# Performance work log

Hardware: AMD Instinct MI355X
Metric: run time of the kernel (lower is better)

## Reference

```python
import jax, jax.numpy as jnp
import numpy as np

# --- Instant-NGP hash-grid constants (from __init__ defaults) ---
T = 2 ** 19          # hash table size per level
NLEVELS = 16
F = 2                # features per level
L = 4                # dir positional-encoding frequencies
LEVELS = np.geomspace(16, 2048, NLEVELS, dtype=int)            # grid resolutions
PRIMES = jnp.array([1, 2654435761, 805459861], dtype=jnp.uint32)
FREQS = (2.0 ** np.arange(L)).astype(np.float32)
# corner c in 0..7 -> bit b_i = use ceil along dim i (matches torch corner order)
BITS = jnp.array([[(c >> i) & 1 for i in range(3)] for c in range(8)], dtype=bool)  # (8,3)


def _hash_encode(pos, table):
    """pos: (P,3) level-scaled positions; table: (T,F). Returns (P,F).
    Spatial hash + gather + trilinear interpolation (== grid_sample trick)."""
    fl = jnp.floor(pos)
    ce = jnp.ceil(pos)
    frac = pos - fl                                             # (P,3) in [0,1)
    corners = jnp.where(BITS[None], ce[:, None, :], fl[:, None, :]).astype(jnp.int32)  # (P,8,3)
    # uint32 wrap-around arithmetic matches torch int64 mod 2^19 (T is a power of 2)
    v = corners.astype(jnp.uint32) * PRIMES                     # (P,8,3)
    h = (v[..., 0] ^ v[..., 1] ^ v[..., 2]) & jnp.uint32(T - 1) # (P,8)
    cf = table[h]                                               # (P,8,F) irregular gather
    w = jnp.prod(jnp.where(BITS[None], frac[:, None, :], 1.0 - frac[:, None, :]), axis=-1)  # (P,8)
    return jnp.einsum('pc,pcf->pf', w, cf)


def setup_inputs() -> dict:
    key = jax.random.key(0)
    ks = jax.random.split(key, 16)
    N, S = 2048, 192
    # positions s.t. x*scene_scale + 0.5 lies mostly in (0,1), a few outside (mask path)
    x = (jax.random.uniform(ks[0], (N, S, 3), jnp.float32) - 0.5) * 1.1
    r_dir = jax.random.normal(ks[1], (N, S, 3), jnp.float32)
    tables = jax.random.normal(ks[2], (NLEVELS, T, F), jnp.float32) * 1e-4

    def lin(k, fan_in, fan_out):
        return jax.random.normal(k, (fan_in, fan_out), jnp.float32) / np.float32(np.sqrt(fan_in))

    din = F * NLEVELS              # 32
    cin = 16 + 3 + 3 * L * 2       # 43
    return {
        'x': x, 'r_dir': r_dir, 'tables': tables,
        'dW1': lin(ks[3], din, 64), 'db1': jnp.zeros((64,), jnp.float32),
        'dW2': lin(ks[4], 64, 16), 'db2': jnp.zeros((16,), jnp.float32),
        'cW1': lin(ks[5], cin, 64), 'cb1': jnp.zeros((64,), jnp.float32),
        'cW2': lin(ks[6], 64, 64), 'cb2': jnp.zeros((64,), jnp.float32),
        'cW3': lin(ks[7], 64, 3), 'cb3': jnp.zeros((3,), jnp.float32),
    }


def reference(x, r_dir, tables, dW1, db1, dW2, db2, cW1, cb1, cW2, cb2, cW3, cb3):
    scene_scale = 1.0
    N, S = x.shape[0], r_dir.shape[1]
    xf = x.reshape(-1, 3) * scene_scale + 0.5          # (P,3)
    rd = r_dir.reshape(-1, 3)                          # (P,3)
    mask = jnp.all(xf > 0, axis=-1) & jnp.all(xf < 1, axis=-1)  # (P,)

    # multi-resolution hash encoding (fixed 16-level loop, vectorized over points)
    feats = jnp.concatenate(
        [_hash_encode(xf * np.float32(LEVELS[i]), tables[i]) for i in range(NLEVELS)],
        axis=-1)                                       # (P, F*NLEVELS)

    log_sigma = jax.nn.relu(feats @ dW1 + db1) @ dW2 + db2        # (P,16)

    # direction positional encoding: [dir, sin(2^l*2pi*dir), cos(...)] -> (P, 3+3*2L)
    xin = rd[..., None] * (2.0 * np.pi * jnp.asarray(FREQS))      # (P,3,L)
    enc = jnp.concatenate([jnp.sin(xin), jnp.cos(xin)], axis=-1).reshape(rd.shape[0], -1)
    enc_dir = jnp.concatenate([rd, enc], axis=-1)                 # (P,27)

    h = jax.nn.relu(jnp.concatenate([log_sigma, enc_dir], axis=-1) @ cW1 + cb1)
    h = jax.nn.relu(h @ cW2 + cb2)
    color = jax.nn.sigmoid(h @ cW3 + cb3)                         # (P,3)

    color = jnp.where(mask[:, None], color, 0.0)
    sigma = jnp.where(mask[:, None], jnp.exp(log_sigma[:, :1]), 0.0)
    return color.reshape(N, S, 3), sigma.reshape(N, S, 1)
```

## Files before the change

kernel.cpp:

```cpp
#include <hip/hip_runtime.h>
#include <hip/hip_bf16.h>
#include <cstdint>

#define NPTS (2048 * 192)
#define TBL  (1u << 19)
#define TMASK (TBL - 1u)
#define PBLOCKS (NPTS / 256)
#define ENC_BLOCKS (PBLOCKS * 16)
#define PREP_BLOCKS 6
#define MLP_BLOCKS 768
#define P2 2654435761u
#define P3 805459861u

__constant__ float LVLS[16] = {16.f, 22.f, 30.f, 42.f, 58.f, 80.f, 111.f, 153.f,
                               212.f, 294.f, 406.f, 561.f, 776.f, 1072.f, 1482.f, 2048.f};

__device__ __forceinline__ uint32_t f2bf(float f) {
    uint32_t u = __float_as_uint(f);
    return (u + 0x7FFFu + ((u >> 16) & 1u)) >> 16;
}
__device__ __forceinline__ uint32_t pack2(float a, float b) {
    return f2bf(a) | (f2bf(b) << 16);
}

#if __has_builtin(__builtin_amdgcn_sinf)
#define SIN_REV(x) __builtin_amdgcn_sinf(x)
#define COS_REV(x) __builtin_amdgcn_cosf(x)
#else
#define SIN_REV(x) __sinf(6.28318530717958647f * (x))
#define COS_REV(x) __cosf(6.28318530717958647f * (x))
#endif

typedef __attribute__((ext_vector_type(8))) short bf16x8;
typedef __attribute__((ext_vector_type(4))) float f32x4;

#define MFMA_BF16 __builtin_amdgcn_mfma_f32_16x16x32_bf16

__global__ __launch_bounds__(256) void k_encode(const float* __restrict__ x,
                                                const float* __restrict__ tables,
                                                uint32_t* __restrict__ feats,
                                                const float* __restrict__ dW1,
                                                const float* __restrict__ dW2,
                                                const float* __restrict__ cW1,
                                                const float* __restrict__ cb1,
                                                const float* __restrict__ cW2,
                                                const float* __restrict__ cW3,
                                                uint4* __restrict__ wfrags)
{
    if (blockIdx.x >= ENC_BLOCKS) {
        int t = (blockIdx.x - ENC_BLOCKS) * 256 + threadIdx.x;
        if (t >= 24 * 64) return;
        int frag = t >> 6, lane = t & 63;
        const float* W; const float* bfold = nullptr;
        int OUT, Kact, Mact, k0, m0;
        if (frag < 4)       { W = dW1; OUT = 64; Kact = 32; Mact = 64; k0 = 0;               m0 = frag * 16; }
        else if (frag < 6)  { W = dW2; OUT = 16; Kact = 64; Mact = 16; k0 = (frag - 4) * 32; m0 = 0; }
        else if (frag < 14) { int i = frag - 6;  W = cW1; OUT = 64; Kact = 43; Mact = 64;
                              k0 = (i & 1) * 32; m0 = (i >> 1) * 16; bfold = cb1; }
        else if (frag < 22) { int i = frag - 14; W = cW2; OUT = 64; Kact = 64; Mact = 64;
                              k0 = (i & 1) * 32; m0 = (i >> 1) * 16; }
        else                { W = cW3; OUT = 3;  Kact = 64; Mact = 3;  k0 = (frag - 22) * 32; m0 = 0; }
        int m  = m0 + (lane & 15);
        int kq = k0 + ((lane >> 4) << 3);
        uint32_t d[4];
#pragma unroll
        for (int j = 0; j < 4; ++j) {
            float a0 = 0.f, a1 = 0.f;
            int ka = kq + 2 * j, kb = ka + 1;
            if (m < Mact) {
                a0 = (ka < Kact) ? W[(size_t)ka * OUT + m]
                                 : ((bfold && ka == Kact) ? bfold[m] : 0.f);
                a1 = (kb < Kact) ? W[(size_t)kb * OUT + m]
                                 : ((bfold && kb == Kact) ? bfold[m] : 0.f);
            }
            d[j] = f2bf(a0) | (f2bf(a1) << 16);
        }
        wfrags[t] = make_uint4(d[0], d[1], d[2], d[3]);
        return;
    }

    int xs   = blockIdx.x & 7;
    int i    = blockIdx.x >> 3;
    int half = i / PBLOCKS;
    int pb   = i - half * PBLOCKS;
    int lvl  = xs + (half << 3);
    int p    = pb * 256 + threadIdx.x;

    size_t p3 = (size_t)p * 3;
    float x0 = x[p3 + 0] + 0.5f;
    float x1 = x[p3 + 1] + 0.5f;
    float x2 = x[p3 + 2] + 0.5f;
    size_t oidx = (size_t)lvl * NPTS + p;

    bool m = (x0 > 0.f) && (x0 < 1.f) && (x1 > 0.f) && (x1 < 1.f) &&
             (x2 > 0.f) && (x2 < 1.f);
    if (!m) { feats[oidx] = 0u; return; }

    float s  = LVLS[lvl];
    float px = x0 * s, py = x1 * s, pz = x2 * s;
    float flx = floorf(px), fly = floorf(py), flz = floorf(pz);
    float frx = px - flx,   fry = py - fly,   frz = pz - flz;
    int ix = (int)flx, iy = (int)fly, iz = (int)flz;
    uint32_t ux = (uint32_t)ix, uy = (uint32_t)iy, uz = (uint32_t)iz;

    uint32_t base[4];
    base[0] = (uy * P2) ^ (uz * P3);
    base[1] = ((uy + 1u) * P2) ^ (uz * P3);
    base[2] = (uy * P2) ^ ((uz + 1u) * P3);
    base[3] = ((uy + 1u) * P2) ^ ((uz + 1u) * P3);

    const float2* tb = (const float2*)tables + (size_t)lvl * TBL;

    float2 v[8];
    if ((ix & 1) == 0) {
        const float4* tb4 = (const float4*)tb;
#pragma unroll
        for (int cc = 0; cc < 4; ++cc) {
            uint32_t h0 = (base[cc] ^ ux) & TMASK;
            float4 qv = tb4[h0 >> 1];
            bool hi = (h0 & 1u) != 0u;
            float2 e0 = hi ? make_float2(qv.z, qv.w) : make_float2(qv.x, qv.y);
            float2 e1 = hi ? make_float2(qv.x, qv.y) : make_float2(qv.z, qv.w);
            v[(cc << 1)]     = e0;
            v[(cc << 1) | 1] = e1;
        }
    } else {
        uint32_t h[8];
#pragma unroll
        for (int c = 0; c < 8; ++c)
            h[c] = (base[c >> 1] ^ (ux + (uint32_t)(c & 1))) & TMASK;
#pragma unroll
        for (int c = 0; c < 8; ++c) v[c] = tb[h[c]];
    }

    float f0 = 0.f, f1 = 0.f;
#pragma unroll
    for (int c = 0; c < 8; ++c) {
        float w = ((c & 1)        ? frx : 1.f - frx)
                * (((c >> 1) & 1) ? fry : 1.f - fry)
                * (((c >> 2) & 1) ? frz : 1.f - frz);
        f0 += w * v[c].x;
        f1 += w * v[c].y;
    }
    feats[oidx] = pack2(f0, f1);
}

__device__ __forceinline__ bf16x8 trans_frag(uint32_t p01a, uint32_t p23a,
                                             uint32_t p01b, uint32_t p23b, int lane)
{
    int q = lane >> 4, col = lane & 15;
    int srcA = (((q & 1) << 1) << 4) | col;
    int srcB = srcA + 16;
    uint32_t a0 = (uint32_t)__shfl((int)p01a, srcA, 64);
    uint32_t b0 = (uint32_t)__shfl((int)p01b, srcA, 64);
    uint32_t a1 = (uint32_t)__shfl((int)p23a, srcA, 64);
    uint32_t b1 = (uint32_t)__shfl((int)p23b, srcA, 64);
    uint32_t a2 = (uint32_t)__shfl((int)p01a, srcB, 64);
    uint32_t b2 = (uint32_t)__shfl((int)p01b, srcB, 64);
    uint32_t a3 = (uint32_t)__shfl((int)p23a, srcB, 64);
    uint32_t b3 = (uint32_t)__shfl((int)p23b, srcB, 64);
    bool hi = q >= 2;
    union { bf16x8 v; uint32_t d[4]; } u;
    u.d[0] = hi ? b0 : a0;
    u.d[1] = hi ? b1 : a1;
    u.d[2] = hi ? b2 : a2;
    u.d[3] = hi ? b3 : a3;
    return u.v;
}

__device__ __forceinline__ float pe_val(int r, float rx, float ry, float rz)
{
    int t = r - 19;
    int d = t >> 3;
    int s = t & 7;
    float comp = (d == 0) ? rx : ((d == 1) ? ry : rz);
    float a  = ldexpf(comp, s & 3);
    float sv = SIN_REV(a);
    float cv = COS_REV(a);
    float v  = (s < 4) ? sv : cv;
    if (r == 16) v = rx;
    if (r == 17) v = ry;
    if (r == 18) v = rz;
    if (r == 43) v = 1.0f;
    if (r > 43)  v = 0.0f;
    return v;
}

__global__ __launch_bounds__(256) void k_mlp(const uint32_t* __restrict__ feats,
                                             const uint4* __restrict__ wfrags,
                                             const float* __restrict__ x,
                                             const float* __restrict__ rdir,
                                             const float* __restrict__ db1,
                                             const float* __restrict__ db2,
                                             const float* __restrict__ cb2,
                                             const float* __restrict__ cb3,
                                             float* __restrict__ out)
{
    int lane = threadIdx.x & 63;
    int q = lane >> 4, col = lane & 15;
    int wgid = blockIdx.x * 4 + (threadIdx.x >> 6);

    union { bf16x8 v; uint4 u; } wf;
    bf16x8 A1[4], A2[2], A3[4][2], A4[4][2], A5[2];
#pragma unroll
    for (int mt = 0; mt < 4; ++mt) { wf.u = wfrags[(0 + mt) * 64 + lane]; A1[mt] = wf.v; }
#pragma unroll
    for (int kt = 0; kt < 2; ++kt) { wf.u = wfrags[(4 + kt) * 64 + lane]; A2[kt] = wf.v; }
#pragma unroll
    for (int mt = 0; mt < 4; ++mt)
#pragma unroll
        for (int kt = 0; kt < 2; ++kt) {
            wf.u = wfrags[(6 + 2 * mt + kt) * 64 + lane];  A3[mt][kt] = wf.v;
            wf.u = wfrags[(14 + 2 * mt + kt) * 64 + lane]; A4[mt][kt] = wf.v;
        }
#pragma unroll
    for (int kt = 0; kt < 2; ++kt) { wf.u = wfrags[(22 + kt) * 64 + lane]; A5[kt] = wf.v; }

    for (int it = 0; it < 8; ++it) {
        int g = (wgid * 8 + it) << 4;
        int pt = g + col;
        size_t pt3 = (size_t)pt * 3;

        union { bf16x8 v; uint32_t d[4]; } Bf;
#pragma unroll
        for (int w = 0; w < 4; ++w)
            Bf.d[w] = feats[(size_t)(q * 4 + w) * NPTS + g + col];

        f32x4 T[4];
#pragma unroll
        for (int mt = 0; mt < 4; ++mt) {
            const float4 bb = *(const float4*)&db1[mt * 16 + q * 4];
            f32x4 c; c[0] = bb.x; c[1] = bb.y; c[2] = bb.z; c[3] = bb.w;
            T[mt] = MFMA_BF16(A1[mt], Bf.v, c, 0, 0, 0);
        }
        uint32_t p01[4], p23[4];
#pragma unroll
        for (int mt = 0; mt < 4; ++mt) {
            p01[mt] = pack2(fmaxf(T[mt][0], 0.f), fmaxf(T[mt][1], 0.f));
            p23[mt] = pack2(fmaxf(T[mt][2], 0.f), fmaxf(T[mt][3], 0.f));
        }
        bf16x8 Bh0 = trans_frag(p01[0], p23[0], p01[1], p23[1], lane);
        bf16x8 Bh1 = trans_frag(p01[2], p23[2], p01[3], p23[3], lane);

        f32x4 Dls;
        {
            const float4 bb = *(const float4*)&db2[q * 4];
            f32x4 c; c[0] = bb.x; c[1] = bb.y; c[2] = bb.z; c[3] = bb.w;
            Dls = MFMA_BF16(A2[0], Bh0, c, 0, 0, 0);
            Dls = MFMA_BF16(A2[1], Bh1, Dls, 0, 0, 0);
        }
        uint32_t lp01 = pack2(Dls[0], Dls[1]);
        uint32_t lp23 = pack2(Dls[2], Dls[3]);

        float rx = rdir[pt3 + 0], ry = rdir[pt3 + 1], rz = rdir[pt3 + 2];

        union { bf16x8 v; uint32_t d[4]; } Ba0, Ba1;
        Ba0.v = trans_frag(lp01, lp23, lp01, lp23, lane);
        {
            int base = q << 3;
#pragma unroll
            for (int j = 0; j < 4; ++j) {
                uint32_t pk = pack2(pe_val(base + 2 * j, rx, ry, rz),
                                    pe_val(base + 2 * j + 1, rx, ry, rz));
                if (q >= 2) Ba0.d[j] = pk;
            }
        }
        {
            int base = 32 + (q << 3);
#pragma unroll
            for (int j = 0; j < 4; ++j)
                Ba1.d[j] = pack2(pe_val(base + 2 * j, rx, ry, rz),
                                 pe_val(base + 2 * j + 1, rx, ry, rz));
        }

        f32x4 C1[4];
#pragma unroll
        for (int mt = 0; mt < 4; ++mt) {
            f32x4 c = {0.f, 0.f, 0.f, 0.f};
            c = MFMA_BF16(A3[mt][0], Ba0.v, c, 0, 0, 0);
            C1[mt] = MFMA_BF16(A3[mt][1], Ba1.v, c, 0, 0, 0);
        }
#pragma unroll
        for (int mt = 0; mt < 4; ++mt) {
            p01[mt] = pack2(fmaxf(C1[mt][0], 0.f), fmaxf(C1[mt][1], 0.f));
            p23[mt] = pack2(fmaxf(C1[mt][2], 0.f), fmaxf(C1[mt][3], 0.f));
        }
        bf16x8 Bc0 = trans_frag(p01[0], p23[0], p01[1], p23[1], lane);
        bf16x8 Bc1 = trans_frag(p01[2], p23[2], p01[3], p23[3], lane);

        f32x4 C2[4];
#pragma unroll
        for (int mt = 0; mt < 4; ++mt) {
            const float4 bb = *(const float4*)&cb2[mt * 16 + q * 4];
            f32x4 c; c[0] = bb.x; c[1] = bb.y; c[2] = bb.z; c[3] = bb.w;
            c = MFMA_BF16(A4[mt][0], Bc0, c, 0, 0, 0);
            C2[mt] = MFMA_BF16(A4[mt][1], Bc1, c, 0, 0, 0);
        }
#pragma unroll
        for (int mt = 0; mt < 4; ++mt) {
            p01[mt] = pack2(fmaxf(C2[mt][0], 0.f), fmaxf(C2[mt][1], 0.f));
            p23[mt] = pack2(fmaxf(C2[mt][2], 0.f), fmaxf(C2[mt][3], 0.f));
        }
        bf16x8 Bd0 = trans_frag(p01[0], p23[0], p01[1], p23[1], lane);
        bf16x8 Bd1 = trans_frag(p01[2], p23[2], p01[3], p23[3], lane);

        f32x4 c5 = {0.f, 0.f, 0.f, 0.f};
        if (q == 0) { c5[0] = cb3[0]; c5[1] = cb3[1]; c5[2] = cb3[2]; }
        f32x4 Dc = MFMA_BF16(A5[0], Bd0, c5, 0, 0, 0);
        Dc = MFMA_BF16(A5[1], Bd1, Dc, 0, 0, 0);

        if (q == 0) {
            float xfx = x[pt3 + 0] + 0.5f;
            float xfy = x[pt3 + 1] + 0.5f;
            float xfz = x[pt3 + 2] + 0.5f;
            bool m = (xfx > 0.f) && (xfx < 1.f) && (xfy > 0.f) && (xfy < 1.f) &&
                     (xfz > 0.f) && (xfz < 1.f);
            out[pt3 + 0] = m ? 1.f / (1.f + __expf(-Dc[0])) : 0.f;
            out[pt3 + 1] = m ? 1.f / (1.f + __expf(-Dc[1])) : 0.f;
            out[pt3 + 2] = m ? 1.f / (1.f + __expf(-Dc[2])) : 0.f;
            out[(size_t)3 * NPTS + pt] = m ? __expf(Dls[0]) : 0.f;
        }
    }
}

extern "C" void kernel_launch(void* const* d_in, const int* in_sizes, int n_in,
                              void* d_out, int out_size, void* d_ws, size_t ws_size,
                              hipStream_t stream) {
    const float* x      = (const float*)d_in[0];
    const float* rdir   = (const float*)d_in[1];
    const float* tables = (const float*)d_in[2];
    const float* dW1 = (const float*)d_in[3];
    const float* db1 = (const float*)d_in[4];
    const float* dW2 = (const float*)d_in[5];
    const float* db2 = (const float*)d_in[6];
    const float* cW1 = (const float*)d_in[7];
    const float* cb1 = (const float*)d_in[8];
    const float* cW2 = (const float*)d_in[9];
    const float* cb2 = (const float*)d_in[10];
    const float* cW3 = (const float*)d_in[11];
    const float* cb3 = (const float*)d_in[12];
    float* out = (float*)d_out;

    uint4*    wfrags = (uint4*)d_ws;
    uint32_t* feats  = (uint32_t*)((char*)d_ws + 32768);

    k_encode<<<ENC_BLOCKS + PREP_BLOCKS, 256, 0, stream>>>(
        x, tables, feats, dW1, dW2, cW1, cb1, cW2, cW3, wfrags);
    k_mlp<<<MLP_BLOCKS, 256, 0, stream>>>(feats, wfrags, x, rdir,
                                          db1, db2, cb2, cb3, out);
}
```

Measured before the change: 256.9 us.

## Truncate bf16 packing with perm, compute cos via shifted sin, double MLP blocks

Replaces round-to-nearest bf16 packing in the MLP kernel with a single byte-permute truncation. The positional-encoding cosine becomes a sine of the argument shifted by a quarter revolution, so each element needs one transcendental instead of two. The MLP grid doubles while each wave handles half as many 16-point groups, which adds parallelism. Truncation adds rounding bias to activations, and the MLP kernel is only part of total time, since the hash-encode gather likely dominates.

```diff
diff --git a/kernel.cpp b/kernel.cpp
--- a/kernel.cpp
+++ b/kernel.cpp
@@ -8,7 +8,7 @@
 #define PBLOCKS (NPTS / 256)
 #define ENC_BLOCKS (PBLOCKS * 16)
 #define PREP_BLOCKS 6
-#define MLP_BLOCKS 768
+#define MLP_BLOCKS 1536
 #define P2 2654435761u
 #define P3 805459861u
 
@@ -22,13 +22,15 @@
 __device__ __forceinline__ uint32_t pack2(float a, float b) {
     return f2bf(a) | (f2bf(b) << 16);
 }
+__device__ __forceinline__ uint32_t pack2t(float a, float b) {
+    return __builtin_amdgcn_perm(__float_as_uint(b), __float_as_uint(a),
+                                 0x07060302u);
+}
 
 #if __has_builtin(__builtin_amdgcn_sinf)
 #define SIN_REV(x) __builtin_amdgcn_sinf(x)
-#define COS_REV(x) __builtin_amdgcn_cosf(x)
 #else
 #define SIN_REV(x) __sinf(6.28318530717958647f * (x))
-#define COS_REV(x) __cosf(6.28318530717958647f * (x))
 #endif
 
 typedef __attribute__((ext_vector_type(8))) short bf16x8;
@@ -174,10 +176,8 @@
     int d = t >> 3;
     int s = t & 7;
     float comp = (d == 0) ? rx : ((d == 1) ? ry : rz);
-    float a  = ldexpf(comp, s & 3);
-    float sv = SIN_REV(a);
-    float cv = COS_REV(a);
-    float v  = (s < 4) ? sv : cv;
+    float a = ldexpf(comp, s & 3) + ((s >= 4) ? 0.25f : 0.0f);
+    float v = SIN_REV(a);
     if (r == 16) v = rx;
     if (r == 17) v = ry;
     if (r == 18) v = rz;
@@ -216,8 +216,8 @@
 #pragma unroll
     for (int kt = 0; kt < 2; ++kt) { wf.u = wfrags[(22 + kt) * 64 + lane]; A5[kt] = wf.v; }
 
-    for (int it = 0; it < 8; ++it) {
-        int g = (wgid * 8 + it) << 4;
+    for (int it = 0; it < 4; ++it) {
+        int g = (wgid * 4 + it) << 4;
         int pt = g + col;
         size_t pt3 = (size_t)pt * 3;
 
@@ -236,8 +236,8 @@
         uint32_t p01[4], p23[4];
 #pragma unroll
         for (int mt = 0; mt < 4; ++mt) {
-            p01[mt] = pack2(fmaxf(T[mt][0], 0.f), fmaxf(T[mt][1], 0.f));
-            p23[mt] = pack2(fmaxf(T[mt][2], 0.f), fmaxf(T[mt][3], 0.f));
+            p01[mt] = pack2t(fmaxf(T[mt][0], 0.f), fmaxf(T[mt][1], 0.f));
+            p23[mt] = pack2t(fmaxf(T[mt][2], 0.f), fmaxf(T[mt][3], 0.f));
         }
         bf16x8 Bh0 = trans_frag(p01[0], p23[0], p01[1], p23[1], lane);
         bf16x8 Bh1 = trans_frag(p01[2], p23[2], p01[3], p23[3], lane);
@@ -249,8 +249,8 @@
             Dls = MFMA_BF16(A2[0], Bh0, c, 0, 0, 0);
             Dls = MFMA_BF16(A2[1], Bh1, Dls, 0, 0, 0);
         }
-        uint32_t lp01 = pack2(Dls[0], Dls[1]);
-        uint32_t lp23 = pack2(Dls[2], Dls[3]);
+        uint32_t lp01 = pack2t(Dls[0], Dls[1]);
+        uint32_t lp23 = pack2t(Dls[2], Dls[3]);
 
         float rx = rdir[pt3 + 0], ry = rdir[pt3 + 1], rz = rdir[pt3 + 2];
 
@@ -260,8 +260,8 @@
             int base = q << 3;
 #pragma unroll
             for (int j = 0; j < 4; ++j) {
-                uint32_t pk = pack2(pe_val(base + 2 * j, rx, ry, rz),
-                                    pe_val(base + 2 * j + 1, rx, ry, rz));
+                uint32_t pk = pack2t(pe_val(base + 2 * j, rx, ry, rz),
+                                     pe_val(base + 2 * j + 1, rx, ry, rz));
                 if (q >= 2) Ba0.d[j] = pk;
             }
         }
@@ -269,8 +269,8 @@
             int base = 32 + (q << 3);
 #pragma unroll
             for (int j = 0; j < 4; ++j)
-                Ba1.d[j] = pack2(pe_val(base + 2 * j, rx, ry, rz),
-                                 pe_val(base + 2 * j + 1, rx, ry, rz));
+                Ba1.d[j] = pack2t(pe_val(base + 2 * j, rx, ry, rz),
+                                  pe_val(base + 2 * j + 1, rx, ry, rz));
         }
 
         f32x4 C1[4];
@@ -282,8 +282,8 @@
         }
 #pragma unroll
         for (int mt = 0; mt < 4; ++mt) {
-            p01[mt] = pack2(fmaxf(C1[mt][0], 0.f), fmaxf(C1[mt][1], 0.f));
-            p23[mt] = pack2(fmaxf(C1[mt][2], 0.f), fmaxf(C1[mt][3], 0.f));
+            p01[mt] = pack2t(fmaxf(C1[mt][0], 0.f), fmaxf(C1[mt][1], 0.f));
+            p23[mt] = pack2t(fmaxf(C1[mt][2], 0.f), fmaxf(C1[mt][3], 0.f));
         }
         bf16x8 Bc0 = trans_frag(p01[0], p23[0], p01[1], p23[1], lane);
         bf16x8 Bc1 = trans_frag(p01[2], p23[2], p01[3], p23[3], lane);
@@ -298,8 +298,8 @@
         }
 #pragma unroll
         for (int mt = 0; mt < 4; ++mt) {
-            p01[mt] = pack2(fmaxf(C2[mt][0], 0.f), fmaxf(C2[mt][1], 0.f));
-            p23[mt] = pack2(fmaxf(C2[mt][2], 0.f), fmaxf(C2[mt][3], 0.f));
+            p01[mt] = pack2t(fmaxf(C2[mt][0], 0.f), fmaxf(C2[mt][1], 0.f));
+            p23[mt] = pack2t(fmaxf(C2[mt][2], 0.f), fmaxf(C2[mt][3], 0.f));
         }
         bf16x8 Bd0 = trans_frag(p01[0], p23[0], p01[1], p23[1], lane);
         bf16x8 Bd1 = trans_frag(p01[2], p23[2], p01[3], p23[3], lane);
```

Result: faster. 248.9 us (-3.1%).
